# Performance work log

Hardware: AMD Instinct MI355X
Metric: run time of the kernel (lower is better)

Reference implementation:

```python
import jax, jax.numpy as jnp
import numpy as np

IN_DIM = 128
D_MODEL = 2 * IN_DIM        # 256, Mamba d_model
D_INNER = 2 * D_MODEL       # 512, expand=2
D_STATE = 16
D_CONV = 4
DT_RANK = (D_MODEL + 15) // 16  # 16
B = 4
C = 1024                    # original channel dim -> Mamba sequence length
EPS = 1e-5


def rmsnorm(x, w):
    return x * jax.lax.rsqrt(jnp.mean(x * x, axis=-1, keepdims=True) + EPS) * w


def conv1x1(x, w, b):
    # x: (B, Cin, L); 1x1 conv == channel matmul
    return jnp.einsum('oi,bil->bol', w, x) + b[None, :, None]


def mamba(u, in_w, conv_w, conv_b, xproj_w, dt_w, dt_b, A_log, Dp, out_w):
    # u: (B, L, D_MODEL) -- faithful mamba_ssm Mamba block (defaults)
    di, K = conv_w.shape
    n = A_log.shape[1]
    r = dt_w.shape[1]
    xz = u @ in_w.T                              # (B,L,2*di)
    xx, z = jnp.split(xz, 2, axis=-1)
    # depthwise causal conv over L
    xt = jnp.pad(jnp.transpose(xx, (0, 2, 1)), ((0, 0), (0, 0), (K - 1, 0)))
    xc = jax.lax.conv_general_dilated(xt, conv_w[:, None, :], (1,), 'VALID',
                                      feature_group_count=di)
    xx = jax.nn.silu(jnp.transpose(xc + conv_b[None, :, None], (0, 2, 1)))
    dbl = xx @ xproj_w.T                         # (B,L,r+2n)
    dt, Bm, Cm = dbl[..., :r], dbl[..., r:r + n], dbl[..., r + n:]
    dt = jax.nn.softplus(dt @ dt_w.T + dt_b)     # (B,L,di)
    A = -jnp.exp(A_log)                          # (di,n)
    dA = jnp.exp(dt[..., None] * A)              # (B,L,di,n)
    dBx = (dt * xx)[..., None] * Bm[:, :, None, :]

    def step(h, inps):
        dA_t, dBx_t, C_t = inps
        h = dA_t * h + dBx_t
        return h, jnp.einsum('bdn,bn->bd', h, C_t)

    h0 = jnp.zeros((u.shape[0], di, n), u.dtype)
    _, ys = jax.lax.scan(step, h0, (jnp.moveaxis(dA, 1, 0),
                                    jnp.moveaxis(dBx, 1, 0),
                                    jnp.moveaxis(Cm, 1, 0)))
    y = jnp.moveaxis(ys, 0, 1) + xx * Dp
    return (y * jax.nn.silu(z)) @ out_w.T


def postnorm_mamba(u, params, norm_w):
    return rmsnorm(mamba(u, *params), norm_w) + u


def _forward(x, W_in, b_in, W_wp, b_wp, W_fp, b_fp, W_bp, b_bp, W_out, b_out,
             norm_w_top,
             f_in_w, f_conv_w, f_conv_b, f_xproj_w, f_dt_w, f_dt_b, f_A_log, f_D, f_out_w, f_norm_w,
             bk_in_w, bk_conv_w, bk_conv_b, bk_xproj_w, bk_dt_w, bk_dt_b, bk_A_log, bk_D, bk_out_w, bk_norm_w):
    residual = x                                  # (B, C, L)
    xn = rmsnorm(x, norm_w_top)                   # RMSNorm over L
    xt = jnp.transpose(xn, (0, 2, 1))             # (B, L, C); L acts as conv channels
    ssm_in = conv1x1(xt, W_in, b_in)              # (B, 2L, C)
    # forward branch
    fwd = conv1x1(ssm_in, W_fp, b_fp)
    fwd = jnp.transpose(fwd, (0, 2, 1))           # (B, C, 2L): Mamba seq=C
    fwd = postnorm_mamba(fwd, (f_in_w, f_conv_w, f_conv_b, f_xproj_w, f_dt_w,
                               f_dt_b, f_A_log, f_D, f_out_w), f_norm_w)
    fwd = jnp.transpose(fwd, (0, 2, 1))           # (B, 2L, C)
    # backward branch (flip along C)
    bwd = conv1x1(ssm_in[:, :, ::-1], W_bp, b_bp)
    bwd = jnp.transpose(bwd, (0, 2, 1))
    bwd = postnorm_mamba(bwd, (bk_in_w, bk_conv_w, bk_conv_b, bk_xproj_w, bk_dt_w,
                               bk_dt_b, bk_A_log, bk_D, bk_out_w), bk_norm_w)
    bwd = jnp.transpose(bwd, (0, 2, 1))[:, :, ::-1]
    # swish gate
    w = conv1x1(xt, W_wp, b_wp)
    w = w * jax.nn.sigmoid(w)
    out = conv1x1(w * fwd + w * bwd, W_out, b_out)  # (B, L, C)
    return jnp.transpose(out, (0, 2, 1)) + residual  # (B, C, L)


def setup_inputs():
    key = jax.random.key(0)
    ks = iter(jax.random.split(key, 64))
    rn = lambda shape, s=0.02: jax.random.normal(next(ks), shape, jnp.float32) * s
    inp = {"x": jax.random.normal(next(ks), (B, C, IN_DIM), jnp.float32)}
    inp["W_in"] = rn((2 * IN_DIM, IN_DIM));   inp["b_in"] = rn((2 * IN_DIM,), 0.1)
    inp["W_wp"] = rn((2 * IN_DIM, IN_DIM));   inp["b_wp"] = rn((2 * IN_DIM,), 0.1)
    inp["W_fp"] = rn((2 * IN_DIM, 2 * IN_DIM)); inp["b_fp"] = rn((2 * IN_DIM,), 0.1)
    inp["W_bp"] = rn((2 * IN_DIM, 2 * IN_DIM)); inp["b_bp"] = rn((2 * IN_DIM,), 0.1)
    inp["W_out"] = rn((IN_DIM, 2 * IN_DIM));  inp["b_out"] = rn((IN_DIM,), 0.1)
    inp["norm_w_top"] = jnp.ones((IN_DIM,), jnp.float32)
    A_init = jnp.log(jnp.broadcast_to(jnp.arange(1, D_STATE + 1, dtype=jnp.float32),
                                      (D_INNER, D_STATE)))
    for p in ("f", "bk"):
        inp[p + "_in_w"] = rn((2 * D_INNER, D_MODEL))
        inp[p + "_conv_w"] = rn((D_INNER, D_CONV), 0.2)
        inp[p + "_conv_b"] = rn((D_INNER,), 0.1)
        inp[p + "_xproj_w"] = rn((DT_RANK + 2 * D_STATE, D_INNER))
        inp[p + "_dt_w"] = rn((D_INNER, DT_RANK), 0.1)
        inp[p + "_dt_b"] = rn((D_INNER,), 0.5)
        inp[p + "_A_log"] = A_init
        inp[p + "_D"] = jnp.ones((D_INNER,), jnp.float32)
        inp[p + "_out_w"] = rn((D_MODEL, D_INNER))
        inp[p + "_norm_w"] = jnp.ones((D_MODEL,), jnp.float32)
    return inp


def reference(x, W_in, b_in, W_wp, b_wp, W_fp, b_fp, W_bp, b_bp, W_out, b_out,
              norm_w_top,
              f_in_w, f_conv_w, f_conv_b, f_xproj_w, f_dt_w, f_dt_b, f_A_log, f_D, f_out_w, f_norm_w,
              bk_in_w, bk_conv_w, bk_conv_b, bk_xproj_w, bk_dt_w, bk_dt_b, bk_A_log, bk_D, bk_out_w, bk_norm_w):
    return _forward(x, W_in, b_in, W_wp, b_wp, W_fp, b_fp, W_bp, b_bp, W_out, b_out,
                    norm_w_top,
                    f_in_w, f_conv_w, f_conv_b, f_xproj_w, f_dt_w, f_dt_b, f_A_log, f_D, f_out_w, f_norm_w,
                    bk_in_w, bk_conv_w, bk_conv_b, bk_xproj_w, bk_dt_w, bk_dt_b, bk_A_log, bk_D, bk_out_w, bk_norm_w)
```

## Files before the change

kernel.cpp:

```cpp
#include <hip/hip_runtime.h>
#include <math.h>

#define C_LEN 1024
#define NROW 4096
#define NCHUNK 32
#define CHUNK 32

typedef __attribute__((ext_vector_type(8))) short short8;
typedef __attribute__((ext_vector_type(4))) float f32x4;

__device__ __forceinline__ float siluf(float x) { return x / (1.f + __expf(-x)); }

__device__ __forceinline__ unsigned short f2bf(float f) {
    unsigned u = __builtin_bit_cast(unsigned, f);
    unsigned r = (u + 0x7FFFu + ((u >> 16) & 1u)) >> 16;
    return (unsigned short)r;
}
__device__ __forceinline__ float bf2f(unsigned short v) {
    unsigned u = ((unsigned)v) << 16;
    return __builtin_bit_cast(float, u);
}

struct WTab {
    const float* s[11];
    unsigned short* d[11];
    int n[11];
};
__global__ __launch_bounds__(256) void k_w2bf(WTab t) {
    int seg = blockIdx.y;
    int n = t.n[seg];
    int i = (blockIdx.x * 256 + threadIdx.x) * 4;
    if (i < n) {
        float4 v = *(const float4*)(t.s[seg] + i);
        unsigned short* o = t.d[seg] + i;
        o[0] = f2bf(v.x); o[1] = f2bf(v.y); o[2] = f2bf(v.z); o[3] = f2bf(v.w);
    }
}

__global__ __launch_bounds__(256) void k_rmsnorm128(const float* __restrict__ x,
                                                    const float* __restrict__ w,
                                                    unsigned short* __restrict__ out) {
    int wave = threadIdx.x >> 6, lane = threadIdx.x & 63;
    int row = blockIdx.x * 4 + wave;
    float2 v = ((const float2*)(x + (size_t)row * 128))[lane];
    float ss = v.x * v.x + v.y * v.y;
    #pragma unroll
    for (int off = 32; off; off >>= 1) ss += __shfl_xor(ss, off, 64);
    float rs = rsqrtf(ss * (1.f / 128.f) + 1e-5f);
    float2 wv = ((const float2*)w)[lane];
    ushort2 o;
    o.x = f2bf(v.x * rs * wv.x);
    o.y = f2bf(v.y * rs * wv.y);
    ((ushort2*)(out + (size_t)row * 128))[lane] = o;
}

__global__ __launch_bounds__(256) void k_gemm_bf(const unsigned short* __restrict__ A,
                                                 const unsigned short* __restrict__ W,
                                                 const float* __restrict__ bias,
                                                 unsigned short* __restrict__ Cbf,
                                                 int N, int K) {
    __shared__ __align__(16) unsigned short As[64 * 72];
    __shared__ __align__(16) unsigned short Bs[64 * 72];
    int tid = threadIdx.x;
    int m0 = blockIdx.y * 64, n0 = blockIdx.x * 64;
    int w = tid >> 6, lane = tid & 63;
    int q = lane >> 4, ln = lane & 15;
    int srow = tid >> 2;
    int sseg = (tid & 3) * 16;

    const unsigned short* pa = A + (size_t)(m0 + srow) * K + sseg;
    const unsigned short* pw = W + (size_t)(n0 + srow) * K + sseg;

    f32x4 acc[4];
    #pragma unroll
    for (int j = 0; j < 4; ++j) acc[j] = (f32x4)(0.f);

    for (int k0 = 0; k0 < K; k0 += 64) {
        *(short8*)&As[srow * 72 + sseg]     = *(const short8*)pa;
        *(short8*)&As[srow * 72 + sseg + 8] = *(const short8*)(pa + 8);
        *(short8*)&Bs[srow * 72 + sseg]     = *(const short8*)pw;
        *(short8*)&Bs[srow * 72 + sseg + 8] = *(const short8*)(pw + 8);
        pa += 64; pw += 64;
        __syncthreads();
        short8 af0 = *(const short8*)&As[(w * 16 + ln) * 72 + q * 8];
        short8 af1 = *(const short8*)&As[(w * 16 + ln) * 72 + 32 + q * 8];
        #pragma unroll
        for (int j = 0; j < 4; ++j) {
            short8 bf0 = *(const short8*)&Bs[(j * 16 + ln) * 72 + q * 8];
            short8 bf1 = *(const short8*)&Bs[(j * 16 + ln) * 72 + 32 + q * 8];
            acc[j] = __builtin_amdgcn_mfma_f32_16x16x32_bf16(af0, bf0, acc[j], 0, 0, 0);
            acc[j] = __builtin_amdgcn_mfma_f32_16x16x32_bf16(af1, bf1, acc[j], 0, 0, 0);
        }
        __syncthreads();
    }
    #pragma unroll
    for (int j = 0; j < 4; ++j) {
        int nn = n0 + j * 16 + ln;
        float bsv = bias[nn];
        #pragma unroll
        for (int r = 0; r < 4; ++r) {
            int m = m0 + w * 16 + q * 4 + r;
            Cbf[(size_t)m * N + nn] = f2bf(acc[j][r] + bsv);
        }
    }
}

__global__ __launch_bounds__(256) void k_gemm3(
        const unsigned short* __restrict__ xn, const unsigned short* __restrict__ ssm,
        const unsigned short* __restrict__ Wfp, const unsigned short* __restrict__ Wbp,
        const unsigned short* __restrict__ Wwp,
        const float* __restrict__ bfp, const float* __restrict__ bbp,
        const float* __restrict__ bwp,
        unsigned short* __restrict__ uf, unsigned short* __restrict__ ub,
        unsigned short* __restrict__ wbuf) {
    __shared__ __align__(16) unsigned short As[64 * 72];
    __shared__ __align__(16) unsigned short Bs[64 * 72];
    int z = blockIdx.z;
    const unsigned short* A = (z == 2) ? xn : ssm;
    const unsigned short* W = (z == 0) ? Wfp : (z == 1) ? Wbp : Wwp;
    const float* bias = (z == 0) ? bfp : (z == 1) ? bbp : bwp;
    unsigned short* C = (z == 0) ? uf : (z == 1) ? ub : wbuf;
    int K = (z == 2) ? 128 : 256;
    int tid = threadIdx.x;
    int m0 = blockIdx.y * 64, n0 = blockIdx.x * 64;
    int w = tid >> 6, lane = tid & 63;
    int q = lane >> 4, ln = lane & 15;
    int srow = tid >> 2;
    int sseg = (tid & 3) * 16;

    int mLog = m0 + srow;
    int mPhys = (z == 1) ? (mLog ^ (C_LEN - 1)) : mLog;
    const unsigned short* pa = A + (size_t)mPhys * K + sseg;
    const unsigned short* pw = W + (size_t)(n0 + srow) * K + sseg;

    f32x4 acc[4];
    #pragma unroll
    for (int j = 0; j < 4; ++j) acc[j] = (f32x4)(0.f);

    for (int k0 = 0; k0 < K; k0 += 64) {
        *(short8*)&As[srow * 72 + sseg]     = *(const short8*)pa;
        *(short8*)&As[srow * 72 + sseg + 8] = *(const short8*)(pa + 8);
        *(short8*)&Bs[srow * 72 + sseg]     = *(const short8*)pw;
        *(short8*)&Bs[srow * 72 + sseg + 8] = *(const short8*)(pw + 8);
        pa += 64; pw += 64;
        __syncthreads();
        short8 af0 = *(const short8*)&As[(w * 16 + ln) * 72 + q * 8];
        short8 af1 = *(const short8*)&As[(w * 16 + ln) * 72 + 32 + q * 8];
        #pragma unroll
        for (int j = 0; j < 4; ++j) {
            short8 bf0 = *(const short8*)&Bs[(j * 16 + ln) * 72 + q * 8];
            short8 bf1 = *(const short8*)&Bs[(j * 16 + ln) * 72 + 32 + q * 8];
            acc[j] = __builtin_amdgcn_mfma_f32_16x16x32_bf16(af0, bf0, acc[j], 0, 0, 0);
            acc[j] = __builtin_amdgcn_mfma_f32_16x16x32_bf16(af1, bf1, acc[j], 0, 0, 0);
        }
        __syncthreads();
    }
    #pragma unroll
    for (int j = 0; j < 4; ++j) {
        int nn = n0 + j * 16 + ln;
        float bsv = bias[nn];
        #pragma unroll
        for (int r = 0; r < 4; ++r) {
            int m = m0 + w * 16 + q * 4 + r;
            float v = acc[j][r] + bsv;
            if (z == 2) v = siluf(v);
            C[(size_t)m * 256 + nn] = f2bf(v);
        }
    }
}

__global__ __launch_bounds__(256) void k_gemm2(
        const unsigned short* __restrict__ A0, const unsigned short* __restrict__ A1,
        const unsigned short* __restrict__ W0, const unsigned short* __restrict__ W1,
        float* __restrict__ Cf0, float* __restrict__ Cf1,
        unsigned short* __restrict__ Cb0, unsigned short* __restrict__ Cb1,
        int N, int K) {
    __shared__ __align__(16) unsigned short As[64 * 72];
    __shared__ __align__(16) unsigned short Bs[64 * 72];
    int p = blockIdx.z;
    const unsigned short* A = p ? A1 : A0;
    const unsigned short* W = p ? W1 : W0;
    float* Cf = p ? Cf1 : Cf0;
    unsigned short* Cbf = p ? Cb1 : Cb0;
    int tid = threadIdx.x;
    int m0 = blockIdx.y * 64, n0 = blockIdx.x * 64;
    int w = tid >> 6, lane = tid & 63;
    int q = lane >> 4, ln = lane & 15;
    int srow = tid >> 2;
    int sseg = (tid & 3) * 16;

    const unsigned short* pa = A + (size_t)(m0 + srow) * K + sseg;
    int nIdx = n0 + srow;
    const unsigned short* pw = W + (size_t)nIdx * K + sseg;
    bool nOK = (nIdx < N);

    f32x4 acc[4];
    #pragma unroll
    for (int j = 0; j < 4; ++j) acc[j] = (f32x4)(0.f);

    for (int k0 = 0; k0 < K; k0 += 64) {
        *(short8*)&As[srow * 72 + sseg]     = *(const short8*)pa;
        *(short8*)&As[srow * 72 + sseg + 8] = *(const short8*)(pa + 8);
        short8 b0 = (short8)(0), b1 = (short8)(0);
        if (nOK) { b0 = *(const short8*)pw; b1 = *(const short8*)(pw + 8); }
        *(short8*)&Bs[srow * 72 + sseg] = b0;
        *(short8*)&Bs[srow * 72 + sseg + 8] = b1;
        pa += 64; pw += 64;
        __syncthreads();
        short8 af0 = *(const short8*)&As[(w * 16 + ln) * 72 + q * 8];
        short8 af1 = *(const short8*)&As[(w * 16 + ln) * 72 + 32 + q * 8];
        #pragma unroll
        for (int j = 0; j < 4; ++j) {
            short8 bf0 = *(const short8*)&Bs[(j * 16 + ln) * 72 + q * 8];
            short8 bf1 = *(const short8*)&Bs[(j * 16 + ln) * 72 + 32 + q * 8];
            acc[j] = __builtin_amdgcn_mfma_f32_16x16x32_bf16(af0, bf0, acc[j], 0, 0, 0);
            acc[j] = __builtin_amdgcn_mfma_f32_16x16x32_bf16(af1, bf1, acc[j], 0, 0, 0);
        }
        __syncthreads();
    }
    #pragma unroll
    for (int j = 0; j < 4; ++j) {
        int nn = n0 + j * 16 + ln;
        if (nn < N) {
            #pragma unroll
            for (int r = 0; r < 4; ++r) {
                int m = m0 + w * 16 + q * 4 + r;
                float v = acc[j][r];
                if (Cf)  Cf[(size_t)m * N + nn] = v;
                if (Cbf) Cbf[(size_t)m * N + nn] = f2bf(v);
            }
        }
    }
}

__global__ __launch_bounds__(256) void k_gemm_comb(const unsigned short* __restrict__ wbuf,
                                                   const unsigned short* __restrict__ mof,
                                                   const unsigned short* __restrict__ mob,
                                                   const unsigned short* __restrict__ W,
                                                   const float* __restrict__ bias,
                                                   const float* __restrict__ resid,
                                                   float* __restrict__ Cf,
                                                   int N, int K) {
    __shared__ __align__(16) unsigned short As[64 * 72];
    __shared__ __align__(16) unsigned short Bs[64 * 72];
    int tid = threadIdx.x;
    int m0 = blockIdx.y * 64, n0 = blockIdx.x * 64;
    int w = tid >> 6, lane = tid & 63;
    int q = lane >> 4, ln = lane & 15;
    int srow = tid >> 2;
    int sseg = (tid & 3) * 16;

    int mLog = m0 + srow;
    int mFlip = mLog ^ (C_LEN - 1);
    int nIdx = n0 + srow;
    const unsigned short* pw = W + (size_t)nIdx * K + sseg;
    bool nOK = (nIdx < N);

    f32x4 acc[4];
    #pragma unroll
    for (int j = 0; j < 4; ++j) acc[j] = (f32x4)(0.f);

    for (int k0 = 0; k0 < K; k0 += 64) {
        size_t off  = (size_t)mLog * 256 + k0 + sseg;
        size_t offb = (size_t)mFlip * 256 + k0 + sseg;
        #pragma unroll
        for (int h = 0; h < 2; ++h) {
            short8 aw = *(const short8*)(wbuf + off + h * 8);
            short8 af = *(const short8*)(mof + off + h * 8);
            short8 ab = *(const short8*)(mob + offb + h * 8);
            short8 av;
            #pragma unroll
            for (int j = 0; j < 8; ++j)
                av[j] = (short)f2bf(bf2f((unsigned short)aw[j]) *
                                    (bf2f((unsigned short)af[j]) + bf2f((unsigned short)ab[j])));
            *(short8*)&As[srow * 72 + sseg + h * 8] = av;
        }
        short8 b0 = (short8)(0), b1 = (short8)(0);
        if (nOK) { b0 = *(const short8*)pw; b1 = *(const short8*)(pw + 8); }
        *(short8*)&Bs[srow * 72 + sseg] = b0;
        *(short8*)&Bs[srow * 72 + sseg + 8] = b1;
        pw += 64;
        __syncthreads();
        short8 af0 = *(const short8*)&As[(w * 16 + ln) * 72 + q * 8];
        short8 af1 = *(const short8*)&As[(w * 16 + ln) * 72 + 32 + q * 8];
        #pragma unroll
        for (int j = 0; j < 4; ++j) {
            short8 bf0 = *(const short8*)&Bs[(j * 16 + ln) * 72 + q * 8];
            short8 bf1 = *(const short8*)&Bs[(j * 16 + ln) * 72 + 32 + q * 8];
            acc[j] = __builtin_amdgcn_mfma_f32_16x16x32_bf16(af0, bf0, acc[j], 0, 0, 0);
            acc[j] = __builtin_amdgcn_mfma_f32_16x16x32_bf16(af1, bf1, acc[j], 0, 0, 0);
        }
        __syncthreads();
    }
    #pragma unroll
    for (int j = 0; j < 4; ++j) {
        int nn = n0 + j * 16 + ln;
        if (nn < N) {
            float bsv = bias[nn];
            #pragma unroll
            for (int r = 0; r < 4; ++r) {
                int m = m0 + w * 16 + q * 4 + r;
                Cf[(size_t)m * N + nn] = acc[j][r] + bsv + resid[(size_t)m * N + nn];
            }
        }
    }
}

__global__ __launch_bounds__(256) void k_conv(const unsigned short* __restrict__ xz0,
                                              const unsigned short* __restrict__ xz1,
                                              const float* __restrict__ cw0,
                                              const float* __restrict__ cw1,
                                              const float* __restrict__ cb0,
                                              const float* __restrict__ cb1,
                                              unsigned short* __restrict__ xc0,
                                              unsigned short* __restrict__ xc1) {
    int pz = blockIdx.z;
    const unsigned short* xz = pz ? xz1 : xz0;
    const float* cw = pz ? cw1 : cw0;
    const float* cb = pz ? cb1 : cb0;
    unsigned short* xconv_bf = pz ? xc1 : xc0;
    int d = blockIdx.x * 256 + threadIdx.x;
    int by = blockIdx.y;
    int b = by >> 6, c0 = (by & 63) * 16;
    float4 cwv = *(const float4*)(cw + d * 4);
    float bias = cb[d];
    const unsigned short* base = xz + (size_t)(b * C_LEN) * 1024 + d;
    float w0 = 0.f, w1 = 0.f, w2 = 0.f;
    if (c0) {
        w0 = bf2f(base[(size_t)(c0 - 3) * 1024]);
        w1 = bf2f(base[(size_t)(c0 - 2) * 1024]);
        w2 = bf2f(base[(size_t)(c0 - 1) * 1024]);
    }
    unsigned short* out = xconv_bf + (size_t)(b * C_LEN + c0) * 512 + d;
    #pragma unroll
    for (int i = 0; i < 16; ++i) {
        float cur = bf2f(base[(size_t)(c0 + i) * 1024]);
        float acc = bias;
        acc = fmaf(cwv.x, w0, acc);
        acc = fmaf(cwv.y, w1, acc);
        acc = fmaf(cwv.z, w2, acc);
        acc = fmaf(cwv.w, cur, acc);
        out[(size_t)i * 512] = f2bf(siluf(acc));
        w0 = w1; w1 = w2; w2 = cur;
    }
}

__global__ __launch_bounds__(256) void k_dtproj(const float* __restrict__ dbl0,
                                                const float* __restrict__ dbl1,
                                                const float* __restrict__ dtw0,
                                                const float* __restrict__ dtw1,
                                                const float* __restrict__ dtb0,
                                                const float* __restrict__ dtb1,
                                                float* __restrict__ dt0,
                                                float* __restrict__ dt1) {
    int pz = blockIdx.z;
    const float* dbl = pz ? dbl1 : dbl0;
    const float* dtw = pz ? dtw1 : dtw0;
    const float* dtb = pz ? dtb1 : dtb0;
    float* dt = pz ? dt1 : dt0;
    int d = blockIdx.x * 256 + threadIdx.x;
    int r0 = blockIdx.y * 8;
    float4 w0 = *(const float4*)(dtw + d * 16);
    float4 w1 = *(const float4*)(dtw + d * 16 + 4);
    float4 w2 = *(const float4*)(dtw + d * 16 + 8);
    float4 w3 = *(const float4*)(dtw + d * 16 + 12);
    float bias = dtb[d];
    #pragma unroll
    for (int rr = 0; rr < 8; ++rr) {
        int r = r0 + rr;
        const float* row = dbl + (size_t)r * 48;
        float s = bias;
        s = fmaf(row[0], w0.x, s);  s = fmaf(row[1], w0.y, s);
        s = fmaf(row[2], w0.z, s);  s = fmaf(row[3], w0.w, s);
        s = fmaf(row[4], w1.x, s);  s = fmaf(row[5], w1.y, s);
        s = fmaf(row[6], w1.z, s);  s = fmaf(row[7], w1.w, s);
        s = fmaf(row[8], w2.x, s);  s = fmaf(row[9], w2.y, s);
        s = fmaf(row[10], w2.z, s); s = fmaf(row[11], w2.w, s);
        s = fmaf(row[12], w3.x, s); s = fmaf(row[13], w3.y, s);
        s = fmaf(row[14], w3.z, s); s = fmaf(row[15], w3.w, s);
        float sp = fmaxf(s, 0.f) + log1pf(__expf(-fabsf(s)));
        dt[(size_t)r * 512 + d] = sp;
    }
}

__global__ __launch_bounds__(256) void k_scan1(const float* __restrict__ dt0,
                                               const float* __restrict__ dt1,
                                               const unsigned short* __restrict__ xc0,
                                               const unsigned short* __restrict__ xc1,
                                               const float* __restrict__ dblA,
                                               const float* __restrict__ dblB,
                                               const float* __restrict__ alog0,
                                               const float* __restrict__ alog1,
                                               float* __restrict__ hfin0,
                                               float* __restrict__ hfin1,
                                               float* __restrict__ Pfin0,
                                               float* __restrict__ Pfin1) {
    int z = blockIdx.z;
    int b = z & 3, p = z >> 2;
    const float* dt = p ? dt1 : dt0;
    const unsigned short* xconv_bf = p ? xc1 : xc0;
    const float* dbl = p ? dblB : dblA;
    const float* A_log = p ? alog1 : alog0;
    float* hfin = p ? hfin1 : hfin0;
    float* Pfin = p ? Pfin1 : Pfin0;
    int tid = threadIdx.x;
    int nh = tid & 1, dl = tid >> 1;
    int k = blockIdx.x, dg = blockIdx.y;
    int d = dg * 128 + dl;
    float4 al0 = *(const float4*)&A_log[d * 16 + nh * 8];
    float4 al1 = *(const float4*)&A_log[d * 16 + nh * 8 + 4];
    float Ac[8] = {-__expf(al0.x), -__expf(al0.y), -__expf(al0.z), -__expf(al0.w),
                   -__expf(al1.x), -__expf(al1.y), -__expf(al1.z), -__expf(al1.w)};
    size_t r0 = (size_t)(b * C_LEN + k * CHUNK);
    const float* pdt = dt + r0 * 512 + d;
    const unsigned short* pxv = xconv_bf + r0 * 512 + d;
    const float* pB  = dbl + r0 * 48 + 16 + nh * 8;
    float h[8] = {0.f, 0.f, 0.f, 0.f, 0.f, 0.f, 0.f, 0.f};
    float sdt = 0.f;
    #pragma unroll 8
    for (int c = 0; c < CHUNK; ++c) {
        float dtv = *pdt;
        float xv  = bf2f(*pxv);
        float4 B0 = *(const float4*)pB;
        float4 B1 = *(const float4*)(pB + 4);
        float dx = dtv * xv;
        float Bv[8] = {B0.x, B0.y, B0.z, B0.w, B1.x, B1.y, B1.z, B1.w};
        #pragma unroll
        for (int j = 0; j < 8; ++j)
            h[j] = fmaf(__expf(dtv * Ac[j]), h[j], dx * Bv[j]);
        sdt += dtv;
        pdt += 512; pxv += 512; pB += 48;
    }
    size_t idx = ((size_t)(b * NCHUNK + k) * 512 + d) * 16 + nh * 8;
    *(float4*)&hfin[idx]     = make_float4(h[0], h[1], h[2], h[3]);
    *(float4*)&hfin[idx + 4] = make_float4(h[4], h[5], h[6], h[7]);
    *(float4*)&Pfin[idx]     = make_float4(__expf(Ac[0] * sdt), __expf(Ac[1] * sdt),
                                           __expf(Ac[2] * sdt), __expf(Ac[3] * sdt));
    *(float4*)&Pfin[idx + 4] = make_float4(__expf(Ac[4] * sdt), __expf(Ac[5] * sdt),
                                           __expf(Ac[6] * sdt), __expf(Ac[7] * sdt));
}

__global__ __launch_bounds__(256) void k_scan2(const float* __restrict__ hfin0,
                                               const float* __restrict__ hfin1,
                                               float* __restrict__ Pfin0,
                                               float* __restrict__ Pfin1) {
    int tt = blockIdx.x * 256 + threadIdx.x;
    int p = tt >> 15;
    int t = tt & 32767;
    const float* hfin = p ? hfin1 : hfin0;
    float* Pfin = p ? Pfin1 : Pfin0;
    int b = t >> 13;
    int dn = t & 8191;
    float carry = 0.f;
    #pragma unroll
    for (int k = 0; k < NCHUNK; ++k) {
        size_t idx = (size_t)(b * NCHUNK + k) * 8192 + dn;
        float pv = Pfin[idx];
        float hf = hfin[idx];
        Pfin[idx] = carry;
        carry = fmaf(pv, carry, hf);
    }
}

__global__ __launch_bounds__(256) void k_scan3(const float* __restrict__ dt0,
                                               const float* __restrict__ dt1,
                                               const unsigned short* __restrict__ xc0,
                                               const unsigned short* __restrict__ xc1,
                                               const float* __restrict__ dblA,
                                               const float* __restrict__ dblB,
                                               const unsigned short* __restrict__ xz0,
                                               const unsigned short* __restrict__ xz1,
                                               const float* __restrict__ alog0,
                                               const float* __restrict__ alog1,
                                               const float* __restrict__ Dp0,
                                               const float* __restrict__ Dp1,
                                               const float* __restrict__ carry0,
                                               const float* __restrict__ carry1,
                                               unsigned short* __restrict__ g0,
                                               unsigned short* __restrict__ g1) {
    int z = blockIdx.z;
    int b = z & 3, p = z >> 2;
    const float* dt = p ? dt1 : dt0;
    const unsigned short* xconv_bf = p ? xc1 : xc0;
    const float* dbl = p ? dblB : dblA;
    const unsigned short* xz = p ? xz1 : xz0;
    const float* A_log = p ? alog1 : alog0;
    const float* Dp = p ? Dp1 : Dp0;
    const float* carryArr = p ? carry1 : carry0;
    unsigned short* gated_bf = p ? g1 : g0;
    int tid = threadIdx.x;
    int nh = tid & 1, dl = tid >> 1;
    int k = blockIdx.x, dg = blockIdx.y;
    int d = dg * 128 + dl;
    float4 al0 = *(const float4*)&A_log[d * 16 + nh * 8];
    float4 al1 = *(const float4*)&A_log[d * 16 + nh * 8 + 4];
    float Ac[8] = {-__expf(al0.x), -__expf(al0.y), -__expf(al0.z), -__expf(al0.w),
                   -__expf(al1.x), -__expf(al1.y), -__expf(al1.z), -__expf(al1.w)};
    float Dd = Dp[d];
    size_t idx = ((size_t)(b * NCHUNK + k) * 512 + d) * 16 + nh * 8;
    float4 h0 = *(const float4*)&carryArr[idx];
    float4 h1 = *(const float4*)&carryArr[idx + 4];
    float h[8] = {h0.x, h0.y, h0.z, h0.w, h1.x, h1.y, h1.z, h1.w};
    size_t r0 = (size_t)(b * C_LEN + k * CHUNK);
    const float* pdt = dt + r0 * 512 + d;
    const unsigned short* pxv = xconv_bf + r0 * 512 + d;
    const float* pB  = dbl + r0 * 48 + 16 + nh * 8;
    const float* pC  = dbl + r0 * 48 + 32 + nh * 8;
    const unsigned short* pz = xz + r0 * 1024 + 512 + d;
    unsigned short* pg = gated_bf + r0 * 512 + d;
    #pragma unroll 4
    for (int c = 0; c < CHUNK; ++c) {
        float dtv = *pdt;
        float xv  = bf2f(*pxv);
        float4 B0 = *(const float4*)pB;
        float4 B1 = *(const float4*)(pB + 4);
        float4 C0 = *(const float4*)pC;
        float4 C1 = *(const float4*)(pC + 4);
        float dx = dtv * xv;
        float Bv[8] = {B0.x, B0.y, B0.z, B0.w, B1.x, B1.y, B1.z, B1.w};
        float Cv[8] = {C0.x, C0.y, C0.z, C0.w, C1.x, C1.y, C1.z, C1.w};
        float contrib = 0.f;
        #pragma unroll
        for (int j = 0; j < 8; ++j) {
            h[j] = fmaf(__expf(dtv * Ac[j]), h[j], dx * Bv[j]);
            contrib = fmaf(h[j], Cv[j], contrib);
        }
        contrib += __shfl_xor(contrib, 1, 64);
        if (nh == 0) {
            float y = contrib + xv * Dd;
            float zv = bf2f(*pz);
            *pg = f2bf(y * siluf(zv));
        }
        pdt += 512; pxv += 512; pB += 48; pC += 48; pz += 1024; pg += 512;
    }
}

__global__ __launch_bounds__(256) void k_postnorm(const unsigned short* __restrict__ mo0,
                                                  const unsigned short* __restrict__ mo1,
                                                  const float* __restrict__ w0,
                                                  const float* __restrict__ w1,
                                                  const unsigned short* __restrict__ u0,
                                                  const unsigned short* __restrict__ u1,
                                                  unsigned short* __restrict__ o0,
                                                  unsigned short* __restrict__ o1) {
    __shared__ float red[4];
    int p = blockIdx.y;
    const unsigned short* mo = p ? mo1 : mo0;
    const float* w = p ? w1 : w0;
    const unsigned short* u = p ? u1 : u0;
    unsigned short* out = p ? o1 : o0;
    int r = blockIdx.x, tid = threadIdx.x;
    float v = bf2f(mo[(size_t)r * 256 + tid]);
    float ss = v * v;
    #pragma unroll
    for (int off = 32; off; off >>= 1) ss += __shfl_xor(ss, off, 64);
    if ((tid & 63) == 0) red[tid >> 6] = ss;
    __syncthreads();
    float tot = red[0] + red[1] + red[2] + red[3];
    float rs = rsqrtf(tot * (1.f / 256.f) + 1e-5f);
    out[(size_t)r * 256 + tid] = f2bf(v * rs * w[tid] + bf2f(u[(size_t)r * 256 + tid]));
}

extern "C" void kernel_launch(void* const* d_in, const int* in_sizes, int n_in,
                              void* d_out, int out_size, void* d_ws, size_t ws_size,
                              hipStream_t stream) {
    const float* x          = (const float*)d_in[0];
    const float* W_in       = (const float*)d_in[1];
    const float* b_in       = (const float*)d_in[2];
    const float* W_wp       = (const float*)d_in[3];
    const float* b_wp       = (const float*)d_in[4];
    const float* W_fp       = (const float*)d_in[5];
    const float* b_fp       = (const float*)d_in[6];
    const float* W_bp       = (const float*)d_in[7];
    const float* b_bp       = (const float*)d_in[8];
    const float* W_out      = (const float*)d_in[9];
    const float* b_out      = (const float*)d_in[10];
    const float* norm_w_top = (const float*)d_in[11];
    const float* mamba_p[2][10];
    for (int p = 0; p < 2; ++p)
        for (int i = 0; i < 10; ++i)
            mamba_p[p][i] = (const float*)d_in[12 + p * 10 + i];

    float* ws = (float*)d_ws;
    float* dblP[2]  = {ws + 0,       ws + 196608};
    float* dtbP[2]  = {ws + 393216,  ws + 2490368};
    float* hfinP[2] = {ws + 4587520, ws + 5636096};
    float* PfinP[2] = {ws + 6684672, ws + 7733248};

    unsigned short* us = (unsigned short*)(ws + 8781824);
    unsigned short* xn_bf   = us + 0;
    unsigned short* ssm_bf  = us + 524288;
    unsigned short* uf_bf   = us + 1572864;
    unsigned short* ub_bf   = us + 2621440;
    unsigned short* wbuf_bf = us + 3670016;
    unsigned short* xzP[2]  = {us + 4718592,  us + 8912896};
    unsigned short* xcP[2]  = {us + 13107200, us + 15204352};
    unsigned short* gP[2]   = {us + 17301504, us + 19398656};
    unsigned short* moP[2]  = {us + 21495808, us + 22544384};
    unsigned short* mof_bf  = us + 23592960;
    unsigned short* mob_bf  = us + 24641536;
    unsigned short* wb      = us + 25690112;
    unsigned short* wb_W_in  = wb + 0;
    unsigned short* wb_W_wp  = wb + 32768;
    unsigned short* wb_W_fp  = wb + 65536;
    unsigned short* wb_W_bp  = wb + 131072;
    unsigned short* wb_W_out = wb + 196608;
    unsigned short* wb_in[2]  = {wb + 229376, wb + 647168};
    unsigned short* wb_xp[2]  = {wb + 491520, wb + 909312};
    unsigned short* wb_outw[2]= {wb + 516096, wb + 933888};

    WTab t;
    t.s[0] = W_in;            t.d[0] = wb_W_in;   t.n[0] = 32768;
    t.s[1] = W_wp;            t.d[1] = wb_W_wp;   t.n[1] = 32768;
    t.s[2] = W_fp;            t.d[2] = wb_W_fp;   t.n[2] = 65536;
    t.s[3] = W_bp;            t.d[3] = wb_W_bp;   t.n[3] = 65536;
    t.s[4] = W_out;           t.d[4] = wb_W_out;  t.n[4] = 32768;
    t.s[5] = mamba_p[0][0];   t.d[5] = wb_in[0];  t.n[5] = 262144;
    t.s[6] = mamba_p[0][3];   t.d[6] = wb_xp[0];  t.n[6] = 24576;
    t.s[7] = mamba_p[0][8];   t.d[7] = wb_outw[0];t.n[7] = 131072;
    t.s[8] = mamba_p[1][0];   t.d[8] = wb_in[1];  t.n[8] = 262144;
    t.s[9] = mamba_p[1][3];   t.d[9] = wb_xp[1];  t.n[9] = 24576;
    t.s[10]= mamba_p[1][8];   t.d[10]= wb_outw[1];t.n[10]= 131072;
    k_w2bf<<<dim3(256, 11), 256, 0, stream>>>(t);

    k_rmsnorm128<<<NROW / 4, 256, 0, stream>>>(x, norm_w_top, xn_bf);
    k_gemm_bf<<<dim3(4, 64), 256, 0, stream>>>(xn_bf, wb_W_in, b_in, ssm_bf, 256, 128);
    k_gemm3<<<dim3(4, 64, 3), 256, 0, stream>>>(xn_bf, ssm_bf, wb_W_fp, wb_W_bp, wb_W_wp,
                                                b_fp, b_bp, b_wp, uf_bf, ub_bf, wbuf_bf);

    k_gemm2<<<dim3(16, 64, 2), 256, 0, stream>>>(uf_bf, ub_bf, wb_in[0], wb_in[1],
                                                 nullptr, nullptr, xzP[0], xzP[1], 1024, 256);
    k_conv<<<dim3(2, 256, 2), 256, 0, stream>>>(xzP[0], xzP[1],
                                                mamba_p[0][1], mamba_p[1][1],
                                                mamba_p[0][2], mamba_p[1][2],
                                                xcP[0], xcP[1]);
    k_gemm2<<<dim3(1, 64, 2), 256, 0, stream>>>(xcP[0], xcP[1], wb_xp[0], wb_xp[1],
                                                dblP[0], dblP[1], nullptr, nullptr, 48, 512);
    k_dtproj<<<dim3(2, 512, 2), 256, 0, stream>>>(dblP[0], dblP[1],
                                                  mamba_p[0][4], mamba_p[1][4],
                                                  mamba_p[0][5], mamba_p[1][5],
                                                  dtbP[0], dtbP[1]);
    k_scan1<<<dim3(NCHUNK, 4, 8), 256, 0, stream>>>(dtbP[0], dtbP[1], xcP[0], xcP[1],
                                                    dblP[0], dblP[1],
                                                    mamba_p[0][6], mamba_p[1][6],
                                                    hfinP[0], hfinP[1], PfinP[0], PfinP[1]);
    k_scan2<<<256, 256, 0, stream>>>(hfinP[0], hfinP[1], PfinP[0], PfinP[1]);
    k_scan3<<<dim3(NCHUNK, 4, 8), 256, 0, stream>>>(dtbP[0], dtbP[1], xcP[0], xcP[1],
                                                    dblP[0], dblP[1], xzP[0], xzP[1],
                                                    mamba_p[0][6], mamba_p[1][6],
                                                    mamba_p[0][7], mamba_p[1][7],
                                                    PfinP[0], PfinP[1], gP[0], gP[1]);
    k_gemm2<<<dim3(4, 64, 2), 256, 0, stream>>>(gP[0], gP[1], wb_outw[0], wb_outw[1],
                                                nullptr, nullptr, moP[0], moP[1], 256, 512);
    k_postnorm<<<dim3(NROW, 2), 256, 0, stream>>>(moP[0], moP[1],
                                                  mamba_p[0][9], mamba_p[1][9],
                                                  uf_bf, ub_bf, mof_bf, mob_bf);

    k_gemm_comb<<<dim3(2, 64), 256, 0, stream>>>(wbuf_bf, mof_bf, mob_bf, wb_W_out, b_out,
                                                 x, (float*)d_out, 128, 256);
}
```

Measured before the change: 266.2 us.

## Fuse weight cast with input norm, conv into x_proj GEMM, postnorm into final GEMM

Folds the top RMSNorm into the weight-conversion launch, so one kernel now does both. The depthwise causal conv+SiLU moves into the x_proj GEMM, which builds the conv output in shared memory and still writes it out for the scan. The postnorm RMS and residual add move into the combining output GEMM, which computes row norms itself before the main loop. This removes three launches and the intermediate mof/mob round trips. In exchange the fused conv GEMM runs only 128 blocks, which limits parallelism, and the final GEMM's prologue recomputes norms per block.

```diff
diff --git a/kernel.cpp b/kernel.cpp
--- a/kernel.cpp
+++ b/kernel.cpp
@@ -26,32 +26,35 @@
     unsigned short* d[11];
     int n[11];
 };
-__global__ __launch_bounds__(256) void k_w2bf(WTab t) {
+__global__ __launch_bounds__(256) void k_prep(WTab t, const float* __restrict__ x,
+                                              const float* __restrict__ nw,
+                                              unsigned short* __restrict__ xn_bf) {
     int seg = blockIdx.y;
-    int n = t.n[seg];
-    int i = (blockIdx.x * 256 + threadIdx.x) * 4;
-    if (i < n) {
-        float4 v = *(const float4*)(t.s[seg] + i);
-        unsigned short* o = t.d[seg] + i;
-        o[0] = f2bf(v.x); o[1] = f2bf(v.y); o[2] = f2bf(v.z); o[3] = f2bf(v.w);
-    }
-}
-
-__global__ __launch_bounds__(256) void k_rmsnorm128(const float* __restrict__ x,
-                                                    const float* __restrict__ w,
-                                                    unsigned short* __restrict__ out) {
-    int wave = threadIdx.x >> 6, lane = threadIdx.x & 63;
-    int row = blockIdx.x * 4 + wave;
-    float2 v = ((const float2*)(x + (size_t)row * 128))[lane];
-    float ss = v.x * v.x + v.y * v.y;
-    #pragma unroll
-    for (int off = 32; off; off >>= 1) ss += __shfl_xor(ss, off, 64);
-    float rs = rsqrtf(ss * (1.f / 128.f) + 1e-5f);
-    float2 wv = ((const float2*)w)[lane];
-    ushort2 o;
-    o.x = f2bf(v.x * rs * wv.x);
-    o.y = f2bf(v.y * rs * wv.y);
-    ((ushort2*)(out + (size_t)row * 128))[lane] = o;
+    if (seg < 11) {
+        int n = t.n[seg];
+        int i = (blockIdx.x * 256 + threadIdx.x) * 4;
+        if (i < n) {
+            float4 v = *(const float4*)(t.s[seg] + i);
+            unsigned short* o = t.d[seg] + i;
+            o[0] = f2bf(v.x); o[1] = f2bf(v.y); o[2] = f2bf(v.z); o[3] = f2bf(v.w);
+        }
+    } else {
+        int wave = threadIdx.x >> 6, lane = threadIdx.x & 63;
+        #pragma unroll
+        for (int it = 0; it < 4; ++it) {
+            int row = blockIdx.x * 16 + it * 4 + wave;
+            float2 v = ((const float2*)(x + (size_t)row * 128))[lane];
+            float ss = v.x * v.x + v.y * v.y;
+            #pragma unroll
+            for (int off = 32; off; off >>= 1) ss += __shfl_xor(ss, off, 64);
+            float rs = rsqrtf(ss * (1.f / 128.f) + 1e-5f);
+            float2 wv = ((const float2*)nw)[lane];
+            ushort2 o;
+            o.x = f2bf(v.x * rs * wv.x);
+            o.y = f2bf(v.y * rs * wv.y);
+            ((ushort2*)(xn_bf + (size_t)row * 128))[lane] = o;
+        }
+    }
 }
 
 __global__ __launch_bounds__(256) void k_gemm_bf(const unsigned short* __restrict__ A,
@@ -172,7 +175,6 @@
 __global__ __launch_bounds__(256) void k_gemm2(
         const unsigned short* __restrict__ A0, const unsigned short* __restrict__ A1,
         const unsigned short* __restrict__ W0, const unsigned short* __restrict__ W1,
-        float* __restrict__ Cf0, float* __restrict__ Cf1,
         unsigned short* __restrict__ Cb0, unsigned short* __restrict__ Cb1,
         int N, int K) {
     __shared__ __align__(16) unsigned short As[64 * 72];
@@ -180,7 +182,6 @@
     int p = blockIdx.z;
     const unsigned short* A = p ? A1 : A0;
     const unsigned short* W = p ? W1 : W0;
-    float* Cf = p ? Cf1 : Cf0;
     unsigned short* Cbf = p ? Cb1 : Cb0;
     int tid = threadIdx.x;
     int m0 = blockIdx.y * 64, n0 = blockIdx.x * 64;
@@ -190,9 +191,7 @@
     int sseg = (tid & 3) * 16;
 
     const unsigned short* pa = A + (size_t)(m0 + srow) * K + sseg;
-    int nIdx = n0 + srow;
-    const unsigned short* pw = W + (size_t)nIdx * K + sseg;
-    bool nOK = (nIdx < N);
+    const unsigned short* pw = W + (size_t)(n0 + srow) * K + sseg;
 
     f32x4 acc[4];
     #pragma unroll
@@ -201,10 +200,8 @@
     for (int k0 = 0; k0 < K; k0 += 64) {
         *(short8*)&As[srow * 72 + sseg]     = *(const short8*)pa;
         *(short8*)&As[srow * 72 + sseg + 8] = *(const short8*)(pa + 8);
-        short8 b0 = (short8)(0), b1 = (short8)(0);
-        if (nOK) { b0 = *(const short8*)pw; b1 = *(const short8*)(pw + 8); }
-        *(short8*)&Bs[srow * 72 + sseg] = b0;
-        *(short8*)&Bs[srow * 72 + sseg + 8] = b1;
+        *(short8*)&Bs[srow * 72 + sseg]     = *(const short8*)pw;
+        *(short8*)&Bs[srow * 72 + sseg + 8] = *(const short8*)(pw + 8);
         pa += 64; pw += 64;
         __syncthreads();
         short8 af0 = *(const short8*)&As[(w * 16 + ln) * 72 + q * 8];
@@ -221,28 +218,120 @@
     #pragma unroll
     for (int j = 0; j < 4; ++j) {
         int nn = n0 + j * 16 + ln;
-        if (nn < N) {
+        #pragma unroll
+        for (int r = 0; r < 4; ++r) {
+            int m = m0 + w * 16 + q * 4 + r;
+            Cbf[(size_t)m * N + nn] = f2bf(acc[j][r]);
+        }
+    }
+}
+
+__global__ __launch_bounds__(256) void k_convdbl(
+        const unsigned short* __restrict__ xz0, const unsigned short* __restrict__ xz1,
+        const unsigned short* __restrict__ W0, const unsigned short* __restrict__ W1,
+        const float* __restrict__ cw0, const float* __restrict__ cw1,
+        const float* __restrict__ cb0, const float* __restrict__ cb1,
+        unsigned short* __restrict__ xc0, unsigned short* __restrict__ xc1,
+        float* __restrict__ dbl0, float* __restrict__ dbl1) {
+    __shared__ __align__(16) unsigned short xzt[68 * 72];
+    __shared__ __align__(16) unsigned short As[64 * 72];
+    __shared__ __align__(16) unsigned short Bs[64 * 72];
+    int p = blockIdx.z;
+    const unsigned short* xz = p ? xz1 : xz0;
+    const unsigned short* W  = p ? W1 : W0;
+    const float* cw = p ? cw1 : cw0;
+    const float* cb = p ? cb1 : cb0;
+    unsigned short* xconv = p ? xc1 : xc0;
+    float* dbl = p ? dbl1 : dbl0;
+
+    int tid = threadIdx.x;
+    int m0 = blockIdx.y * 64;
+    int b = m0 >> 10, c0 = m0 & 1023;
+    int w = tid >> 6, lane = tid & 63;
+    int q = lane >> 4, ln = lane & 15;
+    int srow = tid >> 2, sseg = (tid & 3) * 16;
+    int dd = tid & 63, rg = tid >> 6;
+
+    const unsigned short* pw = W + (size_t)srow * 512 + sseg;
+    bool nOK = (srow < 48);
+
+    f32x4 acc[4];
+    #pragma unroll
+    for (int j = 0; j < 4; ++j) acc[j] = (f32x4)(0.f);
+
+    for (int k0 = 0; k0 < 512; k0 += 64) {
+        short8 b0 = (short8)(0), b1 = (short8)(0);
+        if (nOK) { b0 = *(const short8*)pw; b1 = *(const short8*)(pw + 8); }
+        *(short8*)&Bs[srow * 72 + sseg] = b0;
+        *(short8*)&Bs[srow * 72 + sseg + 8] = b1;
+        pw += 64;
+        #pragma unroll
+        for (int i = 0; i < 3; ++i) {
+            int chunk = tid + i * 256;
+            if (chunk < 536) {
+                int row = chunk >> 3, oct = chunk & 7;
+                int c = c0 - 3 + row;
+                short8 v = (short8)(0);
+                if (c >= 0)
+                    v = *(const short8*)(xz + ((size_t)(b * C_LEN + c) * 1024 + k0 + oct * 8));
+                *(short8*)&xzt[row * 72 + oct * 8] = v;
+            }
+        }
+        __syncthreads();
+        float4 cwv = *(const float4*)(cw + (k0 + dd) * 4);
+        float cbv = cb[k0 + dd];
+        #pragma unroll
+        for (int i = 0; i < 16; ++i) {
+            int lc = rg * 16 + i;
+            float a = cbv;
+            a = fmaf(cwv.x, bf2f(xzt[(lc + 0) * 72 + dd]), a);
+            a = fmaf(cwv.y, bf2f(xzt[(lc + 1) * 72 + dd]), a);
+            a = fmaf(cwv.z, bf2f(xzt[(lc + 2) * 72 + dd]), a);
+            a = fmaf(cwv.w, bf2f(xzt[(lc + 3) * 72 + dd]), a);
+            unsigned short bv = f2bf(siluf(a));
+            As[lc * 72 + dd] = bv;
+            xconv[(size_t)(b * C_LEN + c0 + lc) * 512 + k0 + dd] = bv;
+        }
+        __syncthreads();
+        short8 af0 = *(const short8*)&As[(w * 16 + ln) * 72 + q * 8];
+        short8 af1 = *(const short8*)&As[(w * 16 + ln) * 72 + 32 + q * 8];
+        #pragma unroll
+        for (int j = 0; j < 4; ++j) {
+            short8 bf0 = *(const short8*)&Bs[(j * 16 + ln) * 72 + q * 8];
+            short8 bf1 = *(const short8*)&Bs[(j * 16 + ln) * 72 + 32 + q * 8];
+            acc[j] = __builtin_amdgcn_mfma_f32_16x16x32_bf16(af0, bf0, acc[j], 0, 0, 0);
+            acc[j] = __builtin_amdgcn_mfma_f32_16x16x32_bf16(af1, bf1, acc[j], 0, 0, 0);
+        }
+        __syncthreads();
+    }
+    #pragma unroll
+    for (int j = 0; j < 4; ++j) {
+        int nn = j * 16 + ln;
+        if (nn < 48) {
             #pragma unroll
             for (int r = 0; r < 4; ++r) {
                 int m = m0 + w * 16 + q * 4 + r;
-                float v = acc[j][r];
-                if (Cf)  Cf[(size_t)m * N + nn] = v;
-                if (Cbf) Cbf[(size_t)m * N + nn] = f2bf(v);
+                dbl[(size_t)m * 48 + nn] = acc[j][r];
             }
         }
     }
 }
 
 __global__ __launch_bounds__(256) void k_gemm_comb(const unsigned short* __restrict__ wbuf,
-                                                   const unsigned short* __restrict__ mof,
-                                                   const unsigned short* __restrict__ mob,
+                                                   const unsigned short* __restrict__ mo0,
+                                                   const unsigned short* __restrict__ mo1,
+                                                   const unsigned short* __restrict__ uf,
+                                                   const unsigned short* __restrict__ ub,
+                                                   const float* __restrict__ nw0,
+                                                   const float* __restrict__ nw1,
                                                    const unsigned short* __restrict__ W,
                                                    const float* __restrict__ bias,
                                                    const float* __restrict__ resid,
                                                    float* __restrict__ Cf,
-                                                   int N, int K) {
+                                                   int N) {
     __shared__ __align__(16) unsigned short As[64 * 72];
     __shared__ __align__(16) unsigned short Bs[64 * 72];
+    __shared__ float rsA[64], rsB[64], nwA[256], nwB[256];
     int tid = threadIdx.x;
     int m0 = blockIdx.y * 64, n0 = blockIdx.x * 64;
     int w = tid >> 6, lane = tid & 63;
@@ -250,36 +339,73 @@
     int srow = tid >> 2;
     int sseg = (tid & 3) * 16;
 
+    nwA[tid] = nw0[tid];
+    nwB[tid] = nw1[tid];
+    {
+        int r = tid >> 2, s = tid & 3;
+        int m = m0 + r, mf = m ^ (C_LEN - 1);
+        const unsigned short* p0 = mo0 + (size_t)m * 256 + s * 64;
+        const unsigned short* p1 = mo1 + (size_t)mf * 256 + s * 64;
+        float s0 = 0.f, s1 = 0.f;
+        #pragma unroll
+        for (int i = 0; i < 8; ++i) {
+            short8 v0 = *(const short8*)(p0 + i * 8);
+            short8 v1 = *(const short8*)(p1 + i * 8);
+            #pragma unroll
+            for (int j = 0; j < 8; ++j) {
+                float f0 = bf2f((unsigned short)v0[j]);
+                float f1 = bf2f((unsigned short)v1[j]);
+                s0 = fmaf(f0, f0, s0);
+                s1 = fmaf(f1, f1, s1);
+            }
+        }
+        s0 += __shfl_xor(s0, 1, 64); s0 += __shfl_xor(s0, 2, 64);
+        s1 += __shfl_xor(s1, 1, 64); s1 += __shfl_xor(s1, 2, 64);
+        if (s == 0) {
+            rsA[r] = rsqrtf(s0 * (1.f / 256.f) + 1e-5f);
+            rsB[r] = rsqrtf(s1 * (1.f / 256.f) + 1e-5f);
+        }
+    }
+    __syncthreads();
+
     int mLog = m0 + srow;
     int mFlip = mLog ^ (C_LEN - 1);
     int nIdx = n0 + srow;
-    const unsigned short* pw = W + (size_t)nIdx * K + sseg;
+    const unsigned short* pwt = W + (size_t)nIdx * 256 + sseg;
     bool nOK = (nIdx < N);
+    float rs0 = rsA[srow], rs1 = rsB[srow];
 
     f32x4 acc[4];
     #pragma unroll
     for (int j = 0; j < 4; ++j) acc[j] = (f32x4)(0.f);
 
-    for (int k0 = 0; k0 < K; k0 += 64) {
+    for (int k0 = 0; k0 < 256; k0 += 64) {
         size_t off  = (size_t)mLog * 256 + k0 + sseg;
         size_t offb = (size_t)mFlip * 256 + k0 + sseg;
         #pragma unroll
         for (int h = 0; h < 2; ++h) {
-            short8 aw = *(const short8*)(wbuf + off + h * 8);
-            short8 af = *(const short8*)(mof + off + h * 8);
-            short8 ab = *(const short8*)(mob + offb + h * 8);
+            short8 aw  = *(const short8*)(wbuf + off + h * 8);
+            short8 a0m = *(const short8*)(mo0 + off + h * 8);
+            short8 a0u = *(const short8*)(uf + off + h * 8);
+            short8 a1m = *(const short8*)(mo1 + offb + h * 8);
+            short8 a1u = *(const short8*)(ub + offb + h * 8);
             short8 av;
             #pragma unroll
-            for (int j = 0; j < 8; ++j)
-                av[j] = (short)f2bf(bf2f((unsigned short)aw[j]) *
-                                    (bf2f((unsigned short)af[j]) + bf2f((unsigned short)ab[j])));
+            for (int j = 0; j < 8; ++j) {
+                int k = k0 + sseg + h * 8 + j;
+                float pn = bf2f((unsigned short)a0m[j]) * rs0 * nwA[k]
+                         + bf2f((unsigned short)a0u[j])
+                         + bf2f((unsigned short)a1m[j]) * rs1 * nwB[k]
+                         + bf2f((unsigned short)a1u[j]);
+                av[j] = (short)f2bf(bf2f((unsigned short)aw[j]) * pn);
+            }
             *(short8*)&As[srow * 72 + sseg + h * 8] = av;
         }
         short8 b0 = (short8)(0), b1 = (short8)(0);
-        if (nOK) { b0 = *(const short8*)pw; b1 = *(const short8*)(pw + 8); }
+        if (nOK) { b0 = *(const short8*)pwt; b1 = *(const short8*)(pwt + 8); }
         *(short8*)&Bs[srow * 72 + sseg] = b0;
         *(short8*)&Bs[srow * 72 + sseg + 8] = b1;
-        pw += 64;
+        pwt += 64;
         __syncthreads();
         short8 af0 = *(const short8*)&As[(w * 16 + ln) * 72 + q * 8];
         short8 af1 = *(const short8*)&As[(w * 16 + ln) * 72 + 32 + q * 8];
@@ -303,45 +429,6 @@
                 Cf[(size_t)m * N + nn] = acc[j][r] + bsv + resid[(size_t)m * N + nn];
             }
         }
-    }
-}
-
-__global__ __launch_bounds__(256) void k_conv(const unsigned short* __restrict__ xz0,
-                                              const unsigned short* __restrict__ xz1,
-                                              const float* __restrict__ cw0,
-                                              const float* __restrict__ cw1,
-                                              const float* __restrict__ cb0,
-                                              const float* __restrict__ cb1,
-                                              unsigned short* __restrict__ xc0,
-                                              unsigned short* __restrict__ xc1) {
-    int pz = blockIdx.z;
-    const unsigned short* xz = pz ? xz1 : xz0;
-    const float* cw = pz ? cw1 : cw0;
-    const float* cb = pz ? cb1 : cb0;
-    unsigned short* xconv_bf = pz ? xc1 : xc0;
-    int d = blockIdx.x * 256 + threadIdx.x;
-    int by = blockIdx.y;
-    int b = by >> 6, c0 = (by & 63) * 16;
-    float4 cwv = *(const float4*)(cw + d * 4);
-    float bias = cb[d];
-    const unsigned short* base = xz + (size_t)(b * C_LEN) * 1024 + d;
-    float w0 = 0.f, w1 = 0.f, w2 = 0.f;
-    if (c0) {
-        w0 = bf2f(base[(size_t)(c0 - 3) * 1024]);
-        w1 = bf2f(base[(size_t)(c0 - 2) * 1024]);
-        w2 = bf2f(base[(size_t)(c0 - 1) * 1024]);
-    }
-    unsigned short* out = xconv_bf + (size_t)(b * C_LEN + c0) * 512 + d;
-    #pragma unroll
-    for (int i = 0; i < 16; ++i) {
-        float cur = bf2f(base[(size_t)(c0 + i) * 1024]);
-        float acc = bias;
-        acc = fmaf(cwv.x, w0, acc);
-        acc = fmaf(cwv.y, w1, acc);
-        acc = fmaf(cwv.z, w2, acc);
-        acc = fmaf(cwv.w, cur, acc);
-        out[(size_t)i * 512] = f2bf(siluf(acc));
-        w0 = w1; w1 = w2; w2 = cur;
     }
 }
 
@@ -535,32 +622,6 @@
     }
 }
 
-__global__ __launch_bounds__(256) void k_postnorm(const unsigned short* __restrict__ mo0,
-                                                  const unsigned short* __restrict__ mo1,
-                                                  const float* __restrict__ w0,
-                                                  const float* __restrict__ w1,
-                                                  const unsigned short* __restrict__ u0,
-                                                  const unsigned short* __restrict__ u1,
-                                                  unsigned short* __restrict__ o0,
-                                                  unsigned short* __restrict__ o1) {
-    __shared__ float red[4];
-    int p = blockIdx.y;
-    const unsigned short* mo = p ? mo1 : mo0;
-    const float* w = p ? w1 : w0;
-    const unsigned short* u = p ? u1 : u0;
-    unsigned short* out = p ? o1 : o0;
-    int r = blockIdx.x, tid = threadIdx.x;
-    float v = bf2f(mo[(size_t)r * 256 + tid]);
-    float ss = v * v;
-    #pragma unroll
-    for (int off = 32; off; off >>= 1) ss += __shfl_xor(ss, off, 64);
-    if ((tid & 63) == 0) red[tid >> 6] = ss;
-    __syncthreads();
-    float tot = red[0] + red[1] + red[2] + red[3];
-    float rs = rsqrtf(tot * (1.f / 256.f) + 1e-5f);
-    out[(size_t)r * 256 + tid] = f2bf(v * rs * w[tid] + bf2f(u[(size_t)r * 256 + tid]));
-}
-
 extern "C" void kernel_launch(void* const* d_in, const int* in_sizes, int n_in,
                               void* d_out, int out_size, void* d_ws, size_t ws_size,
                               hipStream_t stream) {
@@ -597,8 +658,6 @@
     unsigned short* xcP[2]  = {us + 13107200, us + 15204352};
     unsigned short* gP[2]   = {us + 17301504, us + 19398656};
     unsigned short* moP[2]  = {us + 21495808, us + 22544384};
-    unsigned short* mof_bf  = us + 23592960;
-    unsigned short* mob_bf  = us + 24641536;
     unsigned short* wb      = us + 25690112;
     unsigned short* wb_W_in  = wb + 0;
     unsigned short* wb_W_wp  = wb + 32768;
@@ -621,21 +680,17 @@
     t.s[8] = mamba_p[1][0];   t.d[8] = wb_in[1];  t.n[8] = 262144;
     t.s[9] = mamba_p[1][3];   t.d[9] = wb_xp[1];  t.n[9] = 24576;
     t.s[10]= mamba_p[1][8];   t.d[10]= wb_outw[1];t.n[10]= 131072;
-    k_w2bf<<<dim3(256, 11), 256, 0, stream>>>(t);
-
-    k_rmsnorm128<<<NROW / 4, 256, 0, stream>>>(x, norm_w_top, xn_bf);
+    k_prep<<<dim3(256, 12), 256, 0, stream>>>(t, x, norm_w_top, xn_bf);
+
     k_gemm_bf<<<dim3(4, 64), 256, 0, stream>>>(xn_bf, wb_W_in, b_in, ssm_bf, 256, 128);
     k_gemm3<<<dim3(4, 64, 3), 256, 0, stream>>>(xn_bf, ssm_bf, wb_W_fp, wb_W_bp, wb_W_wp,
                                                 b_fp, b_bp, b_wp, uf_bf, ub_bf, wbuf_bf);
-
     k_gemm2<<<dim3(16, 64, 2), 256, 0, stream>>>(uf_bf, ub_bf, wb_in[0], wb_in[1],
-                                                 nullptr, nullptr, xzP[0], xzP[1], 1024, 256);
-    k_conv<<<dim3(2, 256, 2), 256, 0, stream>>>(xzP[0], xzP[1],
-                                                mamba_p[0][1], mamba_p[1][1],
-                                                mamba_p[0][2], mamba_p[1][2],
-                                                xcP[0], xcP[1]);
-    k_gemm2<<<dim3(1, 64, 2), 256, 0, stream>>>(xcP[0], xcP[1], wb_xp[0], wb_xp[1],
-                                                dblP[0], dblP[1], nullptr, nullptr, 48, 512);
+                                                 xzP[0], xzP[1], 1024, 256);
+    k_convdbl<<<dim3(1, 64, 2), 256, 0, stream>>>(xzP[0], xzP[1], wb_xp[0], wb_xp[1],
+                                                  mamba_p[0][1], mamba_p[1][1],
+                                                  mamba_p[0][2], mamba_p[1][2],
+                                                  xcP[0], xcP[1], dblP[0], dblP[1]);
     k_dtproj<<<dim3(2, 512, 2), 256, 0, stream>>>(dblP[0], dblP[1],
                                                   mamba_p[0][4], mamba_p[1][4],
                                                   mamba_p[0][5], mamba_p[1][5],
@@ -651,11 +706,8 @@
                                                     mamba_p[0][7], mamba_p[1][7],
                                                     PfinP[0], PfinP[1], gP[0], gP[1]);
     k_gemm2<<<dim3(4, 64, 2), 256, 0, stream>>>(gP[0], gP[1], wb_outw[0], wb_outw[1],
-                                                nullptr, nullptr, moP[0], moP[1], 256, 512);
-    k_postnorm<<<dim3(NROW, 2), 256, 0, stream>>>(moP[0], moP[1],
-                                                  mamba_p[0][9], mamba_p[1][9],
-                                                  uf_bf, ub_bf, mof_bf, mob_bf);
-
-    k_gemm_comb<<<dim3(2, 64), 256, 0, stream>>>(wbuf_bf, mof_bf, mob_bf, wb_W_out, b_out,
-                                                 x, (float*)d_out, 128, 256);
-}
+                                                moP[0], moP[1], 256, 512);
+    k_gemm_comb<<<dim3(2, 64), 256, 0, stream>>>(wbuf_bf, moP[0], moP[1], uf_bf, ub_bf,
+                                                 mamba_p[0][9], mamba_p[1][9],
+                                                 wb_W_out, b_out, x, (float*)d_out, 128);
+}
```

Result: slower. 273.3 us (+2.6%).
